# Optimization experiments

Measured on AMD Instinct MI355X. Metric: run time of the kernel, lower is better.

Reference implementation:

```python
import jax, jax.numpy as jnp
import numpy as np

H = 16       # num_heads
D = 128      # head dim (TokenShift requires D in {16,32,64,128})
BASE = 10000.0


def _shift_linear(x, W, Ws):
    # ShiftLinear: linear -> (B,T,H,D), then token_shift mixing current token
    # with previous token using data-dependent per-head weights.
    B, T, _ = x.shape
    y = (x @ W.T).reshape(B, T, H, D)
    p = jax.nn.sigmoid(x @ Ws.T)                      # (B,T,H) prev-token weight
    y_prev = jnp.pad(y, ((0, 0), (1, 0), (0, 0), (0, 0)))[:, :T]  # shift right by 1
    return y * (1.0 - p)[..., None] + y_prev * p[..., None]


def _rope(q, k):
    # Non-interleaved half-rotation, signs exactly as in the torch source:
    # y1 = x1*cos + x2*sin ; y2 = -x1*sin + x2*cos
    T = q.shape[1]
    half = D // 2
    inv = 1.0 / (BASE ** (jnp.arange(0, D, 2, dtype=jnp.float32) / D))  # (half,)
    freqs = jnp.outer(jnp.arange(T, dtype=jnp.float32), inv)            # (T,half)
    cos = jnp.cos(freqs)[None, :, None, :]
    sin = jnp.sin(freqs)[None, :, None, :]
    def rot(x):
        x1, x2 = x[..., :half], x[..., half:]
        return jnp.concatenate([x1 * cos + x2 * sin, -x1 * sin + x2 * cos], axis=-1)
    return rot(q), rot(k)


def setup_inputs() -> dict:
    key = jax.random.key(0)
    ks = jax.random.split(key, 10)
    B, T, C = 2, 2048, 2048
    s = 0.02
    return {
        "x":   jax.random.normal(ks[0], (B, T, C), jnp.float32),
        "Wq":  s * jax.random.normal(ks[1], (C, C), jnp.float32),
        "Wsq": s * jax.random.normal(ks[2], (H, C), jnp.float32),
        "Wk":  s * jax.random.normal(ks[3], (C, C), jnp.float32),
        "Wsk": s * jax.random.normal(ks[4], (H, C), jnp.float32),
        "Wv":  s * jax.random.normal(ks[5], (C, C), jnp.float32),
        "Wsv": s * jax.random.normal(ks[6], (H, C), jnp.float32),
        "Wf":  s * jax.random.normal(ks[7], (H, C), jnp.float32),
        "bf":  s * jax.random.normal(ks[8], (H,), jnp.float32),
        "Wo":  s * jax.random.normal(ks[9], (C, C), jnp.float32),
    }


def reference(x, Wq, Wsq, Wk, Wsk, Wv, Wsv, Wf, bf, Wo):
    B, T, C = x.shape
    q = _shift_linear(x, Wq, Wsq)          # (B,T,H,D)
    k = _shift_linear(x, Wk, Wsk)
    v = _shift_linear(x, Wv, Wsv)
    q, k = _rope(q, k)

    # forget gate: log f_t per head, cumulative log-decay
    logf = jax.nn.log_sigmoid(x @ Wf.T + bf)       # (B,T,H)
    cum = jnp.cumsum(logf, axis=1).transpose(0, 2, 1)  # (B,H,T)

    s = jnp.einsum('bthd,bshd->bhts', q, k) / np.sqrt(D).astype(np.float32)
    # decay bias D_ij = sum_{l=j+1}^{i} log f_l = cum_i - cum_j
    s = s + cum[:, :, :, None] - cum[:, :, None, :]
    causal = jnp.tril(jnp.ones((T, T), dtype=bool))
    s = jnp.where(causal[None, None], s, -jnp.inf)
    p = jax.nn.softmax(s, axis=-1)                 # (B,H,T,T)

    o = jnp.einsum('bhts,bshd->bthd', p, v).reshape(B, T, C)
    return o @ Wo.T
```

## Files before the change

### kernel.cpp

```cpp
#include <hip/hip_runtime.h>
#include <math.h>


typedef __attribute__((ext_vector_type(8))) short  shortx8;
typedef __attribute__((ext_vector_type(4))) float  floatx4;

#define DEV __device__ __forceinline__

DEV unsigned short f2bf(float f) {
    unsigned int u = __builtin_bit_cast(unsigned int, f);
    u += 0x7FFFu + ((u >> 16) & 1u);
    return (unsigned short)(u >> 16);
}
DEV float bf2f(unsigned short s) {
    unsigned int u = ((unsigned int)s) << 16;
    return __builtin_bit_cast(float, u);
}
DEV void async16(void* lds, const void* g) {
    __builtin_amdgcn_global_load_lds(
        (const __attribute__((address_space(1))) unsigned int*)g,
        (__attribute__((address_space(3))) unsigned int*)lds, 16, 0, 0);
}

__global__ void cvt_bf16(const float* __restrict__ in, unsigned short* __restrict__ out, int n8) {
    int i = blockIdx.x * 256 + threadIdx.x;
    if (i >= n8) return;
    float4 u = ((const float4*)in)[2 * i];
    float4 v = ((const float4*)in)[2 * i + 1];
    shortx8 r;
    r[0] = (short)f2bf(u.x); r[1] = (short)f2bf(u.y); r[2] = (short)f2bf(u.z); r[3] = (short)f2bf(u.w);
    r[4] = (short)f2bf(v.x); r[5] = (short)f2bf(v.y); r[6] = (short)f2bf(v.z); r[7] = (short)f2bf(v.w);
    *(shortx8*)(out + (size_t)i * 8) = r;
}

__global__ void build_wcat(const float* __restrict__ Wsq, const float* __restrict__ Wsk,
                           const float* __restrict__ Wsv, const float* __restrict__ Wf,
                           unsigned short* __restrict__ out) {
    int i = blockIdx.x * 256 + threadIdx.x;
    int c8 = i & 255;
    int row = i >> 8;
    const float* src = nullptr;
    if      (row < 16) src = Wsq + (size_t)row * 2048;
    else if (row < 32) src = Wsk + (size_t)(row - 16) * 2048;
    else if (row < 48) src = Wsv + (size_t)(row - 32) * 2048;
    else if (row < 64) src = Wf  + (size_t)(row - 48) * 2048;
    shortx8 r = (shortx8){0,0,0,0,0,0,0,0};
    if (src) {
#pragma unroll
        for (int q = 0; q < 8; ++q) r[q] = (short)f2bf(src[c8 * 8 + q]);
    }
    *(shortx8*)(out + (size_t)i * 8) = r;
}

template <typename OutT>
__global__ __launch_bounds__(256)
void gemm_bt(const unsigned short* __restrict__ A, const unsigned short* __restrict__ B,
             OutT* __restrict__ C, int M, int N, int K) {
    __shared__ __align__(16) unsigned short As[2][128 * 32];
    __shared__ __align__(16) unsigned short Bs[2][128 * 32];
    const int tid  = threadIdx.x;
    const int lane = tid & 63;
    const int w    = tid >> 6;
    const int nwg  = gridDim.x * gridDim.y;
    const int bid0 = blockIdx.y * gridDim.x + blockIdx.x;
    const int bids = (bid0 & 7) * (nwg >> 3) + (bid0 >> 3);
    const int m0   = (bids % gridDim.x) * 128;
    const int n0   = (bids / gridDim.x) * 128;
    const int wr   = (w >> 1) * 64;
    const int wc   = (w & 1) * 64;
    const int l15  = lane & 15, lg = lane >> 4;
    const int nk   = K >> 5;
    const int c0   = w * 64 + lane;

    floatx4 acc[4][4];
#pragma unroll
    for (int i = 0; i < 4; ++i)
#pragma unroll
        for (int j = 0; j < 4; ++j) acc[i][j] = (floatx4){0.f, 0.f, 0.f, 0.f};

#pragma unroll
    for (int t = 0; t < 2; ++t) {
        int c = t * 256 + c0;
        int row = c >> 2, seg = c & 3;
        async16(&As[0][(t * 256 + w * 64) * 8], A + (size_t)(m0 + row) * K + seg * 8);
        async16(&Bs[0][(t * 256 + w * 64) * 8], B + (size_t)(n0 + row) * K + seg * 8);
    }
    int cur = 0;
    for (int kt = 0; kt < nk; ++kt) {
        __syncthreads();
        if (kt + 1 < nk) {
#pragma unroll
            for (int t = 0; t < 2; ++t) {
                int c = t * 256 + c0;
                int row = c >> 2, seg = c & 3;
                async16(&As[cur ^ 1][(t * 256 + w * 64) * 8],
                        A + (size_t)(m0 + row) * K + (kt + 1) * 32 + seg * 8);
                async16(&Bs[cur ^ 1][(t * 256 + w * 64) * 8],
                        B + (size_t)(n0 + row) * K + (kt + 1) * 32 + seg * 8);
            }
        }
        shortx8 af[4], bfr[4];
#pragma unroll
        for (int i = 0; i < 4; ++i) {
            af[i]  = *(const shortx8*)&As[cur][(wr + i * 16 + l15) * 32 + 8 * lg];
            bfr[i] = *(const shortx8*)&Bs[cur][(wc + i * 16 + l15) * 32 + 8 * lg];
        }
#pragma unroll
        for (int i = 0; i < 4; ++i)
#pragma unroll
            for (int j = 0; j < 4; ++j)
                acc[i][j] = __builtin_amdgcn_mfma_f32_16x16x32_bf16(af[i], bfr[j], acc[i][j], 0, 0, 0);
        cur ^= 1;
    }
#pragma unroll
    for (int i = 0; i < 4; ++i)
#pragma unroll
        for (int j = 0; j < 4; ++j)
#pragma unroll
            for (int r = 0; r < 4; ++r) {
                int row = m0 + wr + i * 16 + 4 * lg + r;
                int col = n0 + wc + j * 16 + l15;
                float v = acc[i][j][r];
                if constexpr (sizeof(OutT) == 2) C[(size_t)row * N + col] = (OutT)f2bf(v);
                else                             C[(size_t)row * N + col] = v;
            }
}

__global__ void cumsum_logf(const float* __restrict__ glog, const float* __restrict__ bfv,
                            float* __restrict__ cum) {
    __shared__ float sums[256];
    const int bh = blockIdx.x, b = bh >> 4, h = bh & 15;
    const int tid = threadIdx.x;
    const float bias = bfv[h];
    float v[8];
    float s = 0.f;
#pragma unroll
    for (int i = 0; i < 8; ++i) {
        int t = tid * 8 + i;
        float z = glog[(size_t)(b * 2048 + t) * 128 + 48 + h] + bias;
        float lf = (z >= 0.f) ? -log1pf(__expf(-z)) : (z - log1pf(__expf(z)));
        s += lf;
        v[i] = s;
    }
    sums[tid] = s;
    __syncthreads();
    for (int off = 1; off < 256; off <<= 1) {
        float t = (tid >= off) ? sums[tid - off] : 0.f;
        __syncthreads();
        sums[tid] += t;
        __syncthreads();
    }
    float basep = sums[tid] - s;
#pragma unroll
    for (int i = 0; i < 8; ++i)
        cum[(size_t)bh * 2048 + tid * 8 + i] = basep + v[i];
}

template <bool ROPE>
__global__ void shift_rope(const unsigned short* __restrict__ Y, int ldY, int yoff,
                           const float* __restrict__ glog, int gcol,
                           unsigned short* __restrict__ Out) {
    int gid = blockIdx.x * 256 + threadIdx.x;
    int j = gid & 7;
    int h = (gid >> 3) & 15;
    int t = (gid >> 7) & 2047;
    int b = gid >> 18;
    const unsigned short* yp = Y + (size_t)(b * 2048 + t) * ldY + yoff + h * 128;
    float z  = glog[(size_t)(b * 2048 + t) * 128 + gcol + h];
    float pg = 1.f / (1.f + __expf(-z));
    shortx8 a1 = *(const shortx8*)(yp + j * 8);
    shortx8 a2 = *(const shortx8*)(yp + 64 + j * 8);
    shortx8 b1 = (shortx8){0,0,0,0,0,0,0,0}, b2 = b1;
    if (t > 0) {
        b1 = *(const shortx8*)(yp - ldY + j * 8);
        b2 = *(const shortx8*)(yp - ldY + 64 + j * 8);
    }
    shortx8 o1, o2;
    const float kf = 13.287712379549449f / 64.f;
#pragma unroll
    for (int i = 0; i < 8; ++i) {
        float m1 = bf2f((unsigned short)a1[i]) * (1.f - pg) + bf2f((unsigned short)b1[i]) * pg;
        float m2 = bf2f((unsigned short)a2[i]) * (1.f - pg) + bf2f((unsigned short)b2[i]) * pg;
        float r1, r2;
        if (ROPE) {
            int d = j * 8 + i;
            float inv = exp2f(-(float)d * kf);
            float ang = (float)t * inv;
            float sv, cv;
            sincosf(ang, &sv, &cv);
            r1 =  m1 * cv + m2 * sv;
            r2 = -m1 * sv + m2 * cv;
        } else { r1 = m1; r2 = m2; }
        o1[i] = (short)f2bf(r1);
        o2[i] = (short)f2bf(r2);
    }
    unsigned short* op = Out + (size_t)((b * 16 + h) * 2048 + t) * 128;
    *(shortx8*)(op + j * 8)      = o1;
    *(shortx8*)(op + 64 + j * 8) = o2;
}

__global__ void transpose_v(const unsigned short* __restrict__ V, unsigned short* __restrict__ Vt) {
    __shared__ unsigned short tile[32][33];
    const int bh = blockIdx.z;
    const int t0 = blockIdx.x * 32, d0 = blockIdx.y * 32;
    const int tx = threadIdx.x, ty = threadIdx.y;
#pragma unroll
    for (int i = 0; i < 4; ++i) {
        int row = ty + i * 8;
        tile[row][tx] = V[(size_t)(bh * 2048 + t0 + row) * 128 + d0 + tx];
    }
    __syncthreads();
#pragma unroll
    for (int i = 0; i < 4; ++i) {
        int drow = ty + i * 8;
        Vt[(size_t)(bh * 128 + d0 + drow) * 2048 + t0 + tx] = tile[tx][drow];
    }
}

__global__ __launch_bounds__(512)
void flash_fwd(const unsigned short* __restrict__ Q, const unsigned short* __restrict__ Km,
               const unsigned short* __restrict__ Vt, const float* __restrict__ cum,
               unsigned short* __restrict__ O) {
    __shared__ __align__(16) unsigned short Ks[3][32 * 128];
    __shared__ __align__(16) unsigned short Vs[3][64 * 64];
    __shared__ __align__(16) float          cumLds[2048];
    __shared__ __align__(16) unsigned short Plds[8][16][40];
    const int tid = threadIdx.x, lane = tid & 63, w = tid >> 6;
    const int l15 = lane & 15, lg = lane >> 4;
    const int bh = blockIdx.y, b = bh >> 4, h = bh & 15;
    const int qx = (blockIdx.x + bh) & 15;
    const int q0 = qx * 128;
    const int qr = q0 + w * 16;
    const size_t base = (size_t)bh * (2048 * 128);
    const float isd = 0.08838834764831845f;
    const int ntiles = 4 * qx + 4;
    const int myn0 = ((qr + 15) >> 5) + 1;
    const int myn = myn0 < ntiles ? myn0 : ntiles;

    const int ik = w * 64 + lane;
    const int kr = ik >> 4, kc = ik & 15;
    const unsigned short* ksrc = Km + base + (size_t)kr * 128 + ((kc ^ (kr & 7)) * 8);
    const int vr = ik >> 3, vc = ik & 7;
    const int vcc = vc ^ (vr & 7);
    const unsigned short* vsrc = Vt + (size_t)(bh * 128 + 2 * vr + (vcc >> 2)) * 2048 + (vcc & 3) * 8;

    const int kx = l15 & 7;
    const int vconst = ((l15 >> 1) * 64) + ((((l15 & 1) * 4 + lg) ^ ((l15 >> 1) & 7)) * 8);

    shortx8 aq[4];
#pragma unroll
    for (int kk = 0; kk < 4; ++kk)
        aq[kk] = *(const shortx8*)(Q + base + (size_t)(qr + l15) * 128 + kk * 32 + 8 * lg);
    float cum_t[4];
#pragma unroll
    for (int r = 0; r < 4; ++r) cum_t[r] = cum[bh * 2048 + qr + 4 * lg + r];

    async16(&cumLds[ik * 4], cum + (size_t)bh * 2048 + ik * 4);
    async16(&Ks[0][ik * 8], ksrc);
    async16(&Vs[0][ik * 8], vsrc);
    async16(&Ks[1][ik * 8], ksrc + 32 * 128);
    async16(&Vs[1][ik * 8], vsrc + 32);

    floatx4 oacc[8];
#pragma unroll
    for (int d = 0; d < 8; ++d) oacc[d] = (floatx4){0.f, 0.f, 0.f, 0.f};
    float m[4]  = {-1e30f, -1e30f, -1e30f, -1e30f};
    float ls[4] = {0.f, 0.f, 0.f, 0.f};

    int bc = 0, bi = 2;
    for (int kt = 0; kt < ntiles; ++kt) {
        asm volatile("s_waitcnt vmcnt(2)" ::: "memory");
        __builtin_amdgcn_s_barrier();
        if (kt + 2 < ntiles) {
            async16(&Ks[bi][ik * 8], ksrc + (size_t)(kt + 2) * 32 * 128);
            async16(&Vs[bi][ik * 8], vsrc + (kt + 2) * 32);
        }
        if (kt < myn) {
            const int s0 = kt * 32;
            floatx4 sacc[2];
            sacc[0] = (floatx4){0.f, 0.f, 0.f, 0.f};
            sacc[1] = (floatx4){0.f, 0.f, 0.f, 0.f};
#pragma unroll
            for (int sf = 0; sf < 2; ++sf)
#pragma unroll
                for (int kk = 0; kk < 4; ++kk) {
                    shortx8 bk = *(const shortx8*)&Ks[bc][(sf * 16 + l15) * 128 + (((kk * 4 + lg) ^ kx) * 8)];
                    sacc[sf] = __builtin_amdgcn_mfma_f32_16x16x32_bf16(aq[kk], bk, sacc[sf], 0, 0, 0);
                }
            float cs[2];
#pragma unroll
            for (int sf = 0; sf < 2; ++sf) cs[sf] = cumLds[s0 + sf * 16 + l15];

            float p[2][4];
            float tmax[4] = {-1e30f, -1e30f, -1e30f, -1e30f};
            const bool maskt = (s0 + 31 > qr);
#pragma unroll
            for (int sf = 0; sf < 2; ++sf)
#pragma unroll
                for (int r = 0; r < 4; ++r) {
                    float sv = sacc[sf][r] * isd + cum_t[r] - cs[sf];
                    if (maskt) {
                        int trow = qr + 4 * lg + r;
                        int scol = s0 + sf * 16 + l15;
                        if (scol > trow) sv = -1e30f;
                    }
                    p[sf][r] = sv;
                    tmax[r] = fmaxf(tmax[r], sv);
                }
#pragma unroll
            for (int r = 0; r < 4; ++r) {
                tmax[r] = fmaxf(tmax[r], __shfl_xor(tmax[r], 1));
                tmax[r] = fmaxf(tmax[r], __shfl_xor(tmax[r], 2));
                tmax[r] = fmaxf(tmax[r], __shfl_xor(tmax[r], 4));
                tmax[r] = fmaxf(tmax[r], __shfl_xor(tmax[r], 8));
            }
            float g = tmax[0] - m[0];
            g = fmaxf(g, tmax[1] - m[1]);
            g = fmaxf(g, tmax[2] - m[2]);
            g = fmaxf(g, tmax[3] - m[3]);
            if (!__all(g <= 8.0f)) {
                float scl[4];
#pragma unroll
                for (int r = 0; r < 4; ++r) {
                    float mn = fmaxf(m[r], tmax[r]);
                    scl[r] = __expf(m[r] - mn);
                    m[r] = mn;
                    ls[r] *= scl[r];
                }
#pragma unroll
                for (int d = 0; d < 8; ++d)
#pragma unroll
                    for (int r = 0; r < 4; ++r) oacc[d][r] *= scl[r];
            }
            float rs[4] = {0.f, 0.f, 0.f, 0.f};
#pragma unroll
            for (int sf = 0; sf < 2; ++sf)
#pragma unroll
                for (int r = 0; r < 4; ++r) {
                    float e = __expf(p[sf][r] - m[r]);
                    p[sf][r] = e;
                    rs[r] += e;
                }
#pragma unroll
            for (int r = 0; r < 4; ++r) {
                rs[r] += __shfl_xor(rs[r], 1);
                rs[r] += __shfl_xor(rs[r], 2);
                rs[r] += __shfl_xor(rs[r], 4);
                rs[r] += __shfl_xor(rs[r], 8);
                ls[r] += rs[r];
            }
#pragma unroll
            for (int sf = 0; sf < 2; ++sf)
#pragma unroll
                for (int r = 0; r < 4; ++r)
                    Plds[w][4 * lg + r][sf * 16 + l15] = f2bf(p[sf][r]);
            shortx8 pa = *(const shortx8*)&Plds[w][l15][8 * lg];
#pragma unroll
            for (int d = 0; d < 8; ++d) {
                shortx8 bv = *(const shortx8*)&Vs[bc][d * 512 + vconst];
                oacc[d] = __builtin_amdgcn_mfma_f32_16x16x32_bf16(pa, bv, oacc[d], 0, 0, 0);
            }
        }
        bc = (bc == 2) ? 0 : bc + 1;
        bi = (bi == 2) ? 0 : bi + 1;
    }
#pragma unroll
    for (int r = 0; r < 4; ++r) {
        float inv = 1.f / ls[r];
        int trow = qr + 4 * lg + r;
        size_t ob = (size_t)(b * 2048 + trow) * 2048 + h * 128;
#pragma unroll
        for (int d = 0; d < 8; ++d)
            O[ob + d * 16 + l15] = f2bf(oacc[d][r] * inv);
    }
}

extern "C" void kernel_launch(void* const* d_in, const int* in_sizes, int n_in,
                              void* d_out, int out_size, void* d_ws, size_t ws_size,
                              hipStream_t stream) {
    const float* x   = (const float*)d_in[0];
    const float* Wq  = (const float*)d_in[1];
    const float* Wsq = (const float*)d_in[2];
    const float* Wk  = (const float*)d_in[3];
    const float* Wsk = (const float*)d_in[4];
    const float* Wv  = (const float*)d_in[5];
    const float* Wsv = (const float*)d_in[6];
    const float* Wf  = (const float*)d_in[7];
    const float* bfv = (const float*)d_in[8];
    const float* Wo  = (const float*)d_in[9];
    float* out = (float*)d_out;
    char* ws = (char*)d_ws;

    if (ws_size >= 145489920ull) {
        unsigned short* xb    = (unsigned short*)(ws + 0);
        unsigned short* Wb3   = (unsigned short*)(ws + 16777216);
        unsigned short* wcat  = (unsigned short*)(ws + 41943040);
        float*          glog  = (float*)(ws + 42467328);
        float*          cum   = (float*)(ws + 44564480);
        unsigned short* qbuf  = (unsigned short*)(ws + 44826624);
        unsigned short* kbuf  = (unsigned short*)(ws + 61603840);
        unsigned short* vbuf  = (unsigned short*)(ws + 78381056);
        unsigned short* ybuf3 = (unsigned short*)(ws + 95158272);
        unsigned short* vt    = ybuf3;

        cvt_bf16<<<4096, 256, 0, stream>>>(x, xb, 1048576);
        build_wcat<<<128, 256, 0, stream>>>(Wsq, Wsk, Wsv, Wf, wcat);
        gemm_bt<float><<<dim3(32, 1), 256, 0, stream>>>(xb, wcat, glog, 4096, 128, 2048);
        cumsum_logf<<<32, 256, 0, stream>>>(glog, bfv, cum);

        cvt_bf16<<<2048, 256, 0, stream>>>(Wq, Wb3, 524288);
        cvt_bf16<<<2048, 256, 0, stream>>>(Wk, Wb3 + 4194304, 524288);
        cvt_bf16<<<2048, 256, 0, stream>>>(Wv, Wb3 + 8388608, 524288);
        gemm_bt<unsigned short><<<dim3(32, 48), 256, 0, stream>>>(xb, Wb3, ybuf3, 4096, 6144, 2048);

        shift_rope<true><<<2048, 256, 0, stream>>>(ybuf3, 6144, 0, glog, 0, qbuf);
        shift_rope<true><<<2048, 256, 0, stream>>>(ybuf3, 6144, 2048, glog, 16, kbuf);
        shift_rope<false><<<2048, 256, 0, stream>>>(ybuf3, 6144, 4096, glog, 32, vbuf);
        transpose_v<<<dim3(64, 4, 32), dim3(32, 8), 0, stream>>>(vbuf, vt);

        flash_fwd<<<dim3(16, 32), 512, 0, stream>>>(qbuf, kbuf, vt, cum, xb);

        cvt_bf16<<<2048, 256, 0, stream>>>(Wo, Wb3, 524288);
        gemm_bt<float><<<dim3(32, 16), 256, 0, stream>>>(xb, Wb3, out, 4096, 2048, 2048);
    } else {
        unsigned short* xb   = (unsigned short*)(ws + 0);
        unsigned short* Wb   = (unsigned short*)(ws + 16777216);
        unsigned short* wcat = (unsigned short*)(ws + 25165824);
        float*          glog = (float*)(ws + 25690112);
        float*          cum  = (float*)(ws + 27787264);
        unsigned short* ybuf = (unsigned short*)(ws + 28049408);
        unsigned short* qbuf = (unsigned short*)(ws + 44826624);
        unsigned short* kbuf = (unsigned short*)(ws + 61603840);
        unsigned short* vbuf = (unsigned short*)(ws + 78381056);
        unsigned short* vt   = (unsigned short*)(ws + 95158272);

        cvt_bf16<<<4096, 256, 0, stream>>>(x, xb, 1048576);
        build_wcat<<<128, 256, 0, stream>>>(Wsq, Wsk, Wsv, Wf, wcat);
        gemm_bt<float><<<dim3(32, 1), 256, 0, stream>>>(xb, wcat, glog, 4096, 128, 2048);
        cumsum_logf<<<32, 256, 0, stream>>>(glog, bfv, cum);

        cvt_bf16<<<2048, 256, 0, stream>>>(Wq, Wb, 524288);
        gemm_bt<unsigned short><<<dim3(32, 16), 256, 0, stream>>>(xb, Wb, ybuf, 4096, 2048, 2048);
        shift_rope<true><<<2048, 256, 0, stream>>>(ybuf, 2048, 0, glog, 0, qbuf);

        cvt_bf16<<<2048, 256, 0, stream>>>(Wk, Wb, 524288);
        gemm_bt<unsigned short><<<dim3(32, 16), 256, 0, stream>>>(xb, Wb, ybuf, 4096, 2048, 2048);
        shift_rope<true><<<2048, 256, 0, stream>>>(ybuf, 2048, 0, glog, 16, kbuf);

        cvt_bf16<<<2048, 256, 0, stream>>>(Wv, Wb, 524288);
        gemm_bt<unsigned short><<<dim3(32, 16), 256, 0, stream>>>(xb, Wb, ybuf, 4096, 2048, 2048);
        shift_rope<false><<<2048, 256, 0, stream>>>(ybuf, 2048, 0, glog, 32, vbuf);
        transpose_v<<<dim3(64, 4, 32), dim3(32, 8), 0, stream>>>(vbuf, vt);

        flash_fwd<<<dim3(16, 32), 512, 0, stream>>>(qbuf, kbuf, vt, cum, ybuf);

        cvt_bf16<<<2048, 256, 0, stream>>>(Wo, Wb, 524288);
        gemm_bt<float><<<dim3(32, 16), 256, 0, stream>>>(ybuf, Wb, out, 4096, 2048, 2048);
    }
}
```

Measured before the change: 590.5 us.

## Skip decay-negligible key tiles via norm bound and precompute RoPE table

The shift_rope pass for K now records a per-head maximum key norm. flash_fwd combines that with each wave's maximum query norm (Cauchy-Schwarz) to bound q·k. It then binary-searches the cumulative log-decay for the first key tile that can still contribute more than e^-30 and starts its loop there, so far-past tiles the forget-gate decay has suppressed are never loaded or computed. RoPE cos/sin values are precomputed into a table instead of calling sincosf per element, and the block-to-q-tile swizzle is dropped. The price is an atomic max in the K shift pass, an extra synchronisation and prologue in flash_fwd, and a bounded approximation in the attention output.

```diff
diff --git a/kernel.cpp b/kernel.cpp
--- a/kernel.cpp
+++ b/kernel.cpp
@@ -31,6 +31,16 @@
     r[0] = (short)f2bf(u.x); r[1] = (short)f2bf(u.y); r[2] = (short)f2bf(u.z); r[3] = (short)f2bf(u.w);
     r[4] = (short)f2bf(v.x); r[5] = (short)f2bf(v.y); r[6] = (short)f2bf(v.z); r[7] = (short)f2bf(v.w);
     *(shortx8*)(out + (size_t)i * 8) = r;
+}
+
+__global__ void rope_tab(float2* __restrict__ tab, float* __restrict__ kmaxp) {
+    int i = blockIdx.x * 256 + threadIdx.x;
+    if (i < 32) kmaxp[i] = 0.f;
+    int d = i & 63, t = i >> 6;
+    float inv = exp2f(-(float)d * (13.287712379549449f / 64.f));
+    float sv, cv;
+    sincosf((float)t * inv, &sv, &cv);
+    tab[i] = make_float2(cv, sv);
 }
 
 __global__ void build_wcat(const float* __restrict__ Wsq, const float* __restrict__ Wsk,
@@ -159,6 +169,7 @@
 template <bool ROPE>
 __global__ void shift_rope(const unsigned short* __restrict__ Y, int ldY, int yoff,
                            const float* __restrict__ glog, int gcol,
+                           const float4* __restrict__ tab4, float* __restrict__ kmaxp,
                            unsigned short* __restrict__ Out) {
     int gid = blockIdx.x * 256 + threadIdx.x;
     int j = gid & 7;
@@ -175,25 +186,46 @@
         b1 = *(const shortx8*)(yp - ldY + j * 8);
         b2 = *(const shortx8*)(yp - ldY + 64 + j * 8);
     }
+    float c_[8], s_[8];
+    if (ROPE && tab4) {
+        const float4* tp = tab4 + (size_t)t * 32 + j * 4;
+#pragma unroll
+        for (int k = 0; k < 4; ++k) {
+            float4 v4 = tp[k];
+            c_[2 * k] = v4.x; s_[2 * k] = v4.y;
+            c_[2 * k + 1] = v4.z; s_[2 * k + 1] = v4.w;
+        }
+    }
     shortx8 o1, o2;
+    float n2 = 0.f;
     const float kf = 13.287712379549449f / 64.f;
 #pragma unroll
     for (int i = 0; i < 8; ++i) {
         float m1 = bf2f((unsigned short)a1[i]) * (1.f - pg) + bf2f((unsigned short)b1[i]) * pg;
         float m2 = bf2f((unsigned short)a2[i]) * (1.f - pg) + bf2f((unsigned short)b2[i]) * pg;
+        n2 += m1 * m1 + m2 * m2;
         float r1, r2;
         if (ROPE) {
-            int d = j * 8 + i;
-            float inv = exp2f(-(float)d * kf);
-            float ang = (float)t * inv;
             float sv, cv;
-            sincosf(ang, &sv, &cv);
+            if (tab4) { cv = c_[i]; sv = s_[i]; }
+            else {
+                int d = j * 8 + i;
+                float inv = exp2f(-(float)d * kf);
+                sincosf((float)t * inv, &sv, &cv);
+            }
             r1 =  m1 * cv + m2 * sv;
             r2 = -m1 * sv + m2 * cv;
         } else { r1 = m1; r2 = m2; }
         o1[i] = (short)f2bf(r1);
         o2[i] = (short)f2bf(r2);
     }
+    if (kmaxp) {
+        n2 += __shfl_xor(n2, 1);
+        n2 += __shfl_xor(n2, 2);
+        n2 += __shfl_xor(n2, 4);
+        if (j == 0)
+            atomicMax((int*)(kmaxp + (b * 16 + h)), __float_as_int(n2));
+    }
     unsigned short* op = Out + (size_t)((b * 16 + h) * 2048 + t) * 128;
     *(shortx8*)(op + j * 8)      = o1;
     *(shortx8*)(op + 64 + j * 8) = o2;
@@ -220,15 +252,16 @@
 __global__ __launch_bounds__(512)
 void flash_fwd(const unsigned short* __restrict__ Q, const unsigned short* __restrict__ Km,
                const unsigned short* __restrict__ Vt, const float* __restrict__ cum,
-               unsigned short* __restrict__ O) {
+               const float* __restrict__ kmaxp, unsigned short* __restrict__ O) {
     __shared__ __align__(16) unsigned short Ks[3][32 * 128];
     __shared__ __align__(16) unsigned short Vs[3][64 * 64];
     __shared__ __align__(16) float          cumLds[2048];
     __shared__ __align__(16) unsigned short Plds[8][16][40];
+    __shared__ int wmin[8];
     const int tid = threadIdx.x, lane = tid & 63, w = tid >> 6;
     const int l15 = lane & 15, lg = lane >> 4;
     const int bh = blockIdx.y, b = bh >> 4, h = bh & 15;
-    const int qx = (blockIdx.x + bh) & 15;
+    const int qx = blockIdx.x;
     const int q0 = qx * 128;
     const int qr = q0 + w * 16;
     const size_t base = (size_t)bh * (2048 * 128);
@@ -247,19 +280,56 @@
     const int kx = l15 & 7;
     const int vconst = ((l15 >> 1) * 64) + ((((l15 & 1) * 4 + lg) ^ ((l15 >> 1) & 7)) * 8);
 
+    async16(&cumLds[ik * 4], cum + (size_t)bh * 2048 + ik * 4);
     shortx8 aq[4];
 #pragma unroll
     for (int kk = 0; kk < 4; ++kk)
         aq[kk] = *(const shortx8*)(Q + base + (size_t)(qr + l15) * 128 + kk * 32 + 8 * lg);
+    float kn2 = kmaxp ? kmaxp[bh] : 0.f;
+    asm volatile("s_waitcnt vmcnt(0)" ::: "memory");
+    __syncthreads();
+
     float cum_t[4];
 #pragma unroll
-    for (int r = 0; r < 4; ++r) cum_t[r] = cum[bh * 2048 + qr + 4 * lg + r];
-
-    async16(&cumLds[ik * 4], cum + (size_t)bh * 2048 + ik * 4);
-    async16(&Ks[0][ik * 8], ksrc);
-    async16(&Vs[0][ik * 8], vsrc);
-    async16(&Ks[1][ik * 8], ksrc + 32 * 128);
-    async16(&Vs[1][ik * 8], vsrc + 32);
+    for (int r = 0; r < 4; ++r) cum_t[r] = cumLds[qr + 4 * lg + r];
+
+    int wstart = 0;
+    if (kmaxp) {
+        float qp = 0.f;
+#pragma unroll
+        for (int kk = 0; kk < 4; ++kk)
+#pragma unroll
+            for (int i = 0; i < 8; ++i) {
+                float v = bf2f((unsigned short)aq[kk][i]);
+                qp += v * v;
+            }
+        qp += __shfl_xor(qp, 16);
+        qp += __shfl_xor(qp, 32);
+        float qn2 = qp;
+        qn2 = fmaxf(qn2, __shfl_xor(qn2, 1));
+        qn2 = fmaxf(qn2, __shfl_xor(qn2, 2));
+        qn2 = fmaxf(qn2, __shfl_xor(qn2, 4));
+        qn2 = fmaxf(qn2, __shfl_xor(qn2, 8));
+        float qkb = sqrtf(qn2 * kn2) * isd;
+        float thr = cumLds[qr] + 2.f * qkb + 30.f;
+        int lo = 0, hi = myn - 1;
+        while (lo < hi) {
+            int mid = (lo + hi) >> 1;
+            if (cumLds[32 * mid + 31] > thr) lo = mid + 1; else hi = mid;
+        }
+        wstart = lo;
+    }
+    if (lane == 0) wmin[w] = wstart;
+    __syncthreads();
+    int s0b = wmin[0];
+#pragma unroll
+    for (int i = 1; i < 8; ++i) s0b = min(s0b, wmin[i]);
+
+    const int t2 = (s0b + 1 < ntiles) ? s0b + 1 : s0b;
+    async16(&Ks[0][ik * 8], ksrc + (size_t)s0b * 32 * 128);
+    async16(&Vs[0][ik * 8], vsrc + s0b * 32);
+    async16(&Ks[1][ik * 8], ksrc + (size_t)t2 * 32 * 128);
+    async16(&Vs[1][ik * 8], vsrc + t2 * 32);
 
     floatx4 oacc[8];
 #pragma unroll
@@ -268,14 +338,15 @@
     float ls[4] = {0.f, 0.f, 0.f, 0.f};
 
     int bc = 0, bi = 2;
-    for (int kt = 0; kt < ntiles; ++kt) {
-        asm volatile("s_waitcnt vmcnt(2)" ::: "memory");
+    for (int kt = s0b; kt < ntiles; ++kt) {
+        if (kt + 1 < ntiles) { asm volatile("s_waitcnt vmcnt(2)" ::: "memory"); }
+        else                 { asm volatile("s_waitcnt vmcnt(0)" ::: "memory"); }
         __builtin_amdgcn_s_barrier();
         if (kt + 2 < ntiles) {
             async16(&Ks[bi][ik * 8], ksrc + (size_t)(kt + 2) * 32 * 128);
             async16(&Vs[bi][ik * 8], vsrc + (kt + 2) * 32);
         }
-        if (kt < myn) {
+        if (kt >= wstart && kt < myn) {
             const int s0 = kt * 32;
             floatx4 sacc[2];
             sacc[0] = (floatx4){0.f, 0.f, 0.f, 0.f};
@@ -391,7 +462,7 @@
     float* out = (float*)d_out;
     char* ws = (char*)d_ws;
 
-    if (ws_size >= 145489920ull) {
+    if (ws_size >= 146538880ull) {
         unsigned short* xb    = (unsigned short*)(ws + 0);
         unsigned short* Wb3   = (unsigned short*)(ws + 16777216);
         unsigned short* wcat  = (unsigned short*)(ws + 41943040);
@@ -400,10 +471,13 @@
         unsigned short* qbuf  = (unsigned short*)(ws + 44826624);
         unsigned short* kbuf  = (unsigned short*)(ws + 61603840);
         unsigned short* vbuf  = (unsigned short*)(ws + 78381056);
-        unsigned short* ybuf3 = (unsigned short*)(ws + 95158272);
+        float2*         tab   = (float2*)(ws + 95158272);
+        float*          kmaxb = (float*)(ws + 96206848);
+        unsigned short* ybuf3 = (unsigned short*)(ws + 96207232);
         unsigned short* vt    = ybuf3;
 
         cvt_bf16<<<4096, 256, 0, stream>>>(x, xb, 1048576);
+        rope_tab<<<512, 256, 0, stream>>>(tab, kmaxb);
         build_wcat<<<128, 256, 0, stream>>>(Wsq, Wsk, Wsv, Wf, wcat);
         gemm_bt<float><<<dim3(32, 1), 256, 0, stream>>>(xb, wcat, glog, 4096, 128, 2048);
         cumsum_logf<<<32, 256, 0, stream>>>(glog, bfv, cum);
@@ -413,12 +487,12 @@
         cvt_bf16<<<2048, 256, 0, stream>>>(Wv, Wb3 + 8388608, 524288);
         gemm_bt<unsigned short><<<dim3(32, 48), 256, 0, stream>>>(xb, Wb3, ybuf3, 4096, 6144, 2048);
 
-        shift_rope<true><<<2048, 256, 0, stream>>>(ybuf3, 6144, 0, glog, 0, qbuf);
-        shift_rope<true><<<2048, 256, 0, stream>>>(ybuf3, 6144, 2048, glog, 16, kbuf);
-        shift_rope<false><<<2048, 256, 0, stream>>>(ybuf3, 6144, 4096, glog, 32, vbuf);
+        shift_rope<true><<<2048, 256, 0, stream>>>(ybuf3, 6144, 0,    glog, 0,  (const float4*)tab, nullptr, qbuf);
+        shift_rope<true><<<2048, 256, 0, stream>>>(ybuf3, 6144, 2048, glog, 16, (const float4*)tab, kmaxb,  kbuf);
+        shift_rope<false><<<2048, 256, 0, stream>>>(ybuf3, 6144, 4096, glog, 32, nullptr, nullptr, vbuf);
         transpose_v<<<dim3(64, 4, 32), dim3(32, 8), 0, stream>>>(vbuf, vt);
 
-        flash_fwd<<<dim3(16, 32), 512, 0, stream>>>(qbuf, kbuf, vt, cum, xb);
+        flash_fwd<<<dim3(16, 32), 512, 0, stream>>>(qbuf, kbuf, vt, cum, kmaxb, xb);
 
         cvt_bf16<<<2048, 256, 0, stream>>>(Wo, Wb3, 524288);
         gemm_bt<float><<<dim3(32, 16), 256, 0, stream>>>(xb, Wb3, out, 4096, 2048, 2048);
@@ -441,18 +515,18 @@
 
         cvt_bf16<<<2048, 256, 0, stream>>>(Wq, Wb, 524288);
         gemm_bt<unsigned short><<<dim3(32, 16), 256, 0, stream>>>(xb, Wb, ybuf, 4096, 2048, 2048);
-        shift_rope<true><<<2048, 256, 0, stream>>>(ybuf, 2048, 0, glog, 0, qbuf);
+        shift_rope<true><<<2048, 256, 0, stream>>>(ybuf, 2048, 0, glog, 0, nullptr, nullptr, qbuf);
 
         cvt_bf16<<<2048, 256, 0, stream>>>(Wk, Wb, 524288);
         gemm_bt<unsigned short><<<dim3(32, 16), 256, 0, stream>>>(xb, Wb, ybuf, 4096, 2048, 2048);
-        shift_rope<true><<<2048, 256, 0, stream>>>(ybuf, 2048, 0, glog, 16, kbuf);
+        shift_rope<true><<<2048, 256, 0, stream>>>(ybuf, 2048, 0, glog, 16, nullptr, nullptr, kbuf);
 
         cvt_bf16<<<2048, 256, 0, stream>>>(Wv, Wb, 524288);
         gemm_bt<unsigned short><<<dim3(32, 16), 256, 0, stream>>>(xb, Wb, ybuf, 4096, 2048, 2048);
-        shift_rope<false><<<2048, 256, 0, stream>>>(ybuf, 2048, 0, glog, 32, vbuf);
+        shift_rope<false><<<2048, 256, 0, stream>>>(ybuf, 2048, 0, glog, 32, nullptr, nullptr, vbuf);
         transpose_v<<<dim3(64, 4, 32), dim3(32, 8), 0, stream>>>(vbuf, vt);
 
-        flash_fwd<<<dim3(16, 32), 512, 0, stream>>>(qbuf, kbuf, vt, cum, ybuf);
+        flash_fwd<<<dim3(16, 32), 512, 0, stream>>>(qbuf, kbuf, vt, cum, nullptr, ybuf);
 
         cvt_bf16<<<2048, 256, 0, stream>>>(Wo, Wb, 524288);
         gemm_bt<float><<<dim3(32, 16), 256, 0, stream>>>(ybuf, Wb, out, 4096, 2048, 2048);
```

Measured after the change: 495.9 us. 1.19x faster.
